# Kernel optimization log

Measured on AMD Instinct MI355X. Metric: run time of the kernel, lower is better.

## Reference

```python
import jax, jax.numpy as jnp
import numpy as np

H, HS, C = 16, 64, 1024  # num_heads, head_size, n_embd

def setup_inputs() -> dict:
    key = jax.random.key(0)
    ks = jax.random.split(key, 5)
    B, T = 2, 2048
    s = 1.0 / np.sqrt(C)
    return {
        "x": jax.random.normal(ks[0], (B, T, C), dtype=jnp.float32),
        "Wq": jax.random.normal(ks[1], (H, C, HS), dtype=jnp.float32) * s,
        "Wk": jax.random.normal(ks[2], (H, C, HS), dtype=jnp.float32) * s,
        "Wv": jax.random.normal(ks[3], (H, C, HS), dtype=jnp.float32) * s,
        "Wo": jax.random.normal(ks[4], (C, C), dtype=jnp.float32) * s,
    }

def reference(x, Wq, Wk, Wv, Wo):
    B, T, Cdim = x.shape
    scale = Cdim ** -0.5  # original scales by n_embd**-0.5, not head_size
    q = jnp.einsum('btc,hcd->bhtd', x, Wq)
    k = jnp.einsum('btc,hcd->bhtd', x, Wk)
    v = jnp.einsum('btc,hcd->bhtd', x, Wv)
    wei = jnp.einsum('bhtd,bhsd->bhts', q, k) * scale  # [B,H,T,T]
    causal = jnp.tril(jnp.ones((T, T), dtype=bool))
    wei = jnp.where(causal, wei, -jnp.inf)
    wei = jax.nn.softmax(wei, axis=-1)
    out = jnp.einsum('bhts,bhsd->bhtd', wei, v)  # [B,H,T,HS]
    out = out.transpose(0, 2, 1, 3).reshape(B, T, -1)  # concat heads -> [B,T,C]
    return out @ Wo.T
```

## Files before the change

kernel.cpp:

```cpp
#include <hip/hip_runtime.h>

typedef unsigned short ushort_t;
typedef __bf16 bf16x8 __attribute__((ext_vector_type(8)));
typedef float f32x4 __attribute__((ext_vector_type(4)));
typedef float f32x16 __attribute__((ext_vector_type(16)));
typedef unsigned short ushortx8 __attribute__((ext_vector_type(8)));
typedef unsigned int uintx4 __attribute__((ext_vector_type(4)));

#define NH 16
#define HS 64
#define CD 1024
#define NB 2
#define NT 2048
#define BT (NB * NT)
#define N3 (3 * CD)

#define L2E_DIV32 0.04508422002778011f

#define PART1_OFF 50331648
#define SLOT_BYTES 18432
#define R0_SLOTS 796


__device__ __forceinline__ ushort_t bf16_rne(float f) {
  union { float f; unsigned u; } v; v.f = f;
  unsigned u = v.u;
  unsigned r = (u + 0x7FFFu + ((u >> 16) & 1u)) >> 16;
  return (ushort_t)r;
}

__device__ __forceinline__ float bf2f(ushort_t u) {
  union { unsigned u; float f; } v; v.u = ((unsigned)u) << 16; return v.f;
}

__device__ __forceinline__ void gload_lds16(const ushort_t* g, ushort_t* l) {
  __builtin_amdgcn_global_load_lds(
      (const __attribute__((address_space(1))) unsigned int*)g,
      (__attribute__((address_space(3))) unsigned int*)l, 16, 0, 0);
}

__device__ __forceinline__ f32x4 mfma16(ushortx8 a, ushortx8 b, f32x4 c) {
  return __builtin_amdgcn_mfma_f32_16x16x32_bf16(
      __builtin_bit_cast(bf16x8, a), __builtin_bit_cast(bf16x8, b), c, 0, 0, 0);
}

__device__ __forceinline__ f32x16 mfma32(ushortx8 a, ushortx8 b, f32x16 c) {
  return __builtin_amdgcn_mfma_f32_32x32x16_bf16(
      __builtin_bit_cast(bf16x8, a), __builtin_bit_cast(bf16x8, b), c, 0, 0, 0);
}

__device__ __forceinline__ unsigned cvt_pk_bf16(float lo, float hi) {
  unsigned r;
  asm("v_cvt_pk_bf16_f32 %0, %1, %2" : "=v"(r) : "v"(lo), "v"(hi));
  return r;
}

__device__ __forceinline__ void plswap(unsigned &a, unsigned &b) {
  asm volatile("v_permlane32_swap_b32 %0, %1" : "+v"(a), "+v"(b));
}


__global__ __launch_bounds__(256)
void pack_cast(const float4* __restrict__ in, ushort_t* __restrict__ out, int n4) {
  const int i = blockIdx.x * 256 + threadIdx.x;
  if (i >= n4) return;
  const float4 v = in[i];
  ushort4 r;
  r.x = bf16_rne(v.x); r.y = bf16_rne(v.y);
  r.z = bf16_rne(v.z); r.w = bf16_rne(v.w);
  *(ushort4*)(out + (size_t)i * 4) = r;
}

__global__ __launch_bounds__(256)
void pack_wqkv(const float* __restrict__ Wq, const float* __restrict__ Wk,
               const float* __restrict__ Wv, ushort_t* __restrict__ out) {
  __shared__ ushort_t tile[64 * 66];
  const int sh = blockIdx.y;
  const int s = sh >> 4, h = sh & 15;
  const float* W = (s == 0) ? Wq : ((s == 1) ? Wk : Wv);
  const int c0 = blockIdx.x * 64;
  const int t = threadIdx.x;
#pragma unroll
  for (int j = 0; j < 16; ++j) {
    const int idx = t + j * 256;
    const int ci = idx >> 6, d = idx & 63;
    const float v = W[(size_t)(h * 1024 + c0 + ci) * 64 + d];
    tile[d * 66 + ci] = bf16_rne(v);
  }
  __syncthreads();
#pragma unroll
  for (int j = 0; j < 16; ++j) {
    const int idx = t + j * 256;
    const int d = idx >> 6, ci = idx & 63;
    out[(size_t)(s * 1024 + h * 64 + d) * 1024 + c0 + ci] = tile[d * 66 + ci];
  }
}


template <bool OUT_BF16>
__global__ __launch_bounds__(256)
void gemm_bt(const ushort_t* __restrict__ A, const ushort_t* __restrict__ Bt,
             void* __restrict__ Cv, int M, int N, int K, int qcols) {
  __shared__ __align__(16) ushort_t ldsA[2][128 * 32];
  __shared__ __align__(16) ushort_t ldsB[2][128 * 32];
  const int tid = threadIdx.x;
  const int lane = tid & 63;
  const int wave = tid >> 6;
  const int row0 = blockIdx.y * 128;
  const int col0 = blockIdx.x * 128;
  const int wm = wave >> 1, wn = wave & 1;
  const float sc = (col0 < qcols) ? L2E_DIV32 : 1.0f;

  f32x4 acc[4][4] = {};

  const int ce = (tid & 3) * 8;

  auto stage = [&](int buf, int kt) {
    const int kbase = kt * 32;
#pragma unroll
    for (int j = 0; j < 2; ++j) {
      const int r = j * 64 + (tid >> 2);
      gload_lds16(A + (size_t)(row0 + r) * K + kbase + ce,
                  &ldsA[buf][(j * 256 + wave * 64) * 8]);
      gload_lds16(Bt + (size_t)(col0 + r) * K + kbase + ce,
                  &ldsB[buf][(j * 256 + wave * 64) * 8]);
    }
  };

  const int arow_off = (wm * 64 + (lane & 15)) * 32 + (lane >> 4) * 8;
  const int brow_off = (wn * 64 + (lane & 15)) * 32 + (lane >> 4) * 8;

  auto compute = [&](int buf) {
    ushortx8 af[4], bfr[4];
#pragma unroll
    for (int m = 0; m < 4; ++m)
      af[m] = *(const ushortx8*)&ldsA[buf][arow_off + m * 512];
#pragma unroll
    for (int n = 0; n < 4; ++n)
      bfr[n] = *(const ushortx8*)&ldsB[buf][brow_off + n * 512];
#pragma unroll
    for (int m = 0; m < 4; ++m)
#pragma unroll
      for (int n = 0; n < 4; ++n)
        acc[m][n] = mfma16(af[m], bfr[n], acc[m][n]);
  };

  stage(0, 0);
  __syncthreads();
  const int nk = K >> 5;
  for (int kt = 0; kt < nk; ++kt) {
    const int cur = kt & 1;
    if (kt + 1 < nk) stage(cur ^ 1, kt + 1);
    compute(cur);
    __syncthreads();
  }

#pragma unroll
  for (int m = 0; m < 4; ++m) {
    const int rbase = row0 + wm * 64 + m * 16 + (lane >> 4) * 4;
#pragma unroll
    for (int n = 0; n < 4; ++n) {
      const int col = col0 + wn * 64 + n * 16 + (lane & 15);
#pragma unroll
      for (int i = 0; i < 4; ++i) {
        const size_t off = (size_t)(rbase + i) * N + col;
        if constexpr (OUT_BF16) ((ushort_t*)Cv)[off] = bf16_rne(acc[m][n][i] * sc);
        else                    ((float*)Cv)[off]    = acc[m][n][i] * sc;
      }
    }
  }
}


__global__ __launch_bounds__(256, 4)
void attn_fwd4(const ushort_t* __restrict__ QKV, ushort_t* __restrict__ O,
               char* __restrict__ wsb) {
  __shared__ __align__(16) ushort_t Klds[2][64 * 64];
  __shared__ __align__(16) ushort_t Vlds[2][64 * 64];

  const int tid = threadIdx.x;
  const int lane = tid & 63;
  const int w = tid >> 6;
  const int l31 = lane & 31;
  const int h = lane >> 5;

  const int x = blockIdx.x;
  const int bh = x & 31;
  const int c = x >> 5;
  int qb, j, k;
  if (c < 16)      { qb = 12 + (c >> 2); j = c & 3; k = 4; }
  else if (c < 28) { const int e = c - 16; const int q = e / 3; qb = 8 + q; j = e - q * 3; k = 3; }
  else if (c < 36) { const int e = c - 28; qb = 4 + (e >> 1); j = e & 1; k = 2; }
  else             { qb = c - 36; j = 0; k = 1; }
  const int nt = 2 * qb + 2;
  const int bsz = nt / k, rem = nt - bsz * k;
  const int t0 = j * bsz + (j < rem ? j : rem);
  const int t1 = t0 + bsz + (j < rem ? 1 : 0);
  const bool lastc = (t1 == nt);

  const int b = bh >> 4, head = bh & 15;
  const size_t base = (size_t)b * NT * N3;
  const int qw0 = qb * 128 + w * 32;
  const int qg = qw0 + l31;
  const int tmax = lastc ? (2 * qb + (w >> 1)) : (t1 - 1);

  ushortx8 qf[4];
  {
    const ushort_t* qp = QKV + base + (size_t)qg * N3 + head * 64 + h * 8;
#pragma unroll
    for (int kc = 0; kc < 4; ++kc) qf[kc] = *(const ushortx8*)(qp + kc * 16);
  }

  int koff[4];
#pragma unroll
  for (int kc = 0; kc < 4; ++kc)
    koff[kc] = l31 * 128 + (((2 * kc + h) ^ (l31 & 7)) * 16);

  const int vr = l31, vc = w * 2 + h;
  int voff[8];
#pragma unroll
  for (int e = 0; e < 8; ++e)
    voff[e] = (vc * 8 + e) * 128 + (((vr >> 2) ^ e) * 16) + 4 * (vr & 3);

  const int rowA = tid >> 3, ccA = tid & 7;
  const int rowB = 32 + rowA;
  const ushort_t* kg = QKV + base + 1024 + head * 64;
  const ushort_t* ksA = kg + (size_t)(t0 * 64 + rowA) * N3 + ((ccA ^ (rowA & 7)) * 8);
  const ushort_t* ksB = kg + (size_t)(t0 * 64 + rowB) * N3 + ((ccA ^ (rowB & 7)) * 8);
  const ushort_t* vs  = QKV + base + (size_t)(t0 * 64 + 2 * vr) * N3 + 2048 + head * 64 + vc * 8;
  const size_t tadv = (size_t)64 * N3;

  f32x16 oA = {}, oB = {};
  float m_r = -INFINITY, l_r = 0.f;

  ushortx8 vst0 = *(const ushortx8*)vs;
  ushortx8 vst1 = *(const ushortx8*)(vs + N3);
  gload_lds16(ksA, &Klds[0][(w * 64) * 8]);
  gload_lds16(ksB, &Klds[0][(256 + w * 64) * 8]);
#pragma unroll
  for (int e = 0; e < 8; ++e) {
    ushort2 val; val.x = vst0[e]; val.y = vst1[e];
    *(ushort2*)((char*)&Vlds[0][0] + voff[e]) = val;
  }
  asm volatile("s_waitcnt lgkmcnt(0)" ::: "memory");

  int curb = 0;
  for (int t = t0; t < t1; ++t) {
    const bool hasn = (t + 1 < t1);
    const int nxt = curb ^ 1;
    if (hasn) {
      ksA += tadv; ksB += tadv; vs += tadv;
      vst0 = *(const ushortx8*)vs;
      vst1 = *(const ushortx8*)(vs + N3);
      gload_lds16(ksA, &Klds[nxt][(w * 64) * 8]);
      gload_lds16(ksB, &Klds[nxt][(256 + w * 64) * 8]);
      asm volatile("s_waitcnt vmcnt(4)" ::: "memory");
    } else {
      asm volatile("s_waitcnt vmcnt(0)" ::: "memory");
    }
    __builtin_amdgcn_s_barrier();
    asm volatile("" ::: "memory");

    if (t <= tmax) {
      const bool diag = lastc && (t == tmax);
      const bool halfB = diag && ((w & 1) == 0);
      const char* kb = (const char*)&Klds[curb][0];
      const char* vb = (const char*)&Vlds[curb][0];

      f32x16 sA = {}, sB = {};
#pragma unroll
      for (int kc = 0; kc < 4; ++kc)
        sA = mfma32(*(const ushortx8*)(kb + koff[kc]), qf[kc], sA);
      if (!halfB) {
#pragma unroll
        for (int kc = 0; kc < 4; ++kc)
          sB = mfma32(*(const ushortx8*)(kb + 4096 + koff[kc]), qf[kc], sB);
      }

      if (diag) {
#pragma unroll
        for (int r = 0; r < 16; ++r) {
          const int krow = (r & 3) + 8 * (r >> 2) + 4 * h;
          if (halfB) { if (krow > l31) sA[r] = -INFINITY; }
          else       { if (krow > l31) sB[r] = -INFINITY; }
        }
      }

      float mm[16];
#pragma unroll
      for (int r = 0; r < 16; ++r) mm[r] = halfB ? sA[r] : fmaxf(sA[r], sB[r]);
#pragma unroll
      for (int st = 8; st >= 1; st >>= 1)
#pragma unroll
        for (int r = 0; r < st; ++r) mm[r] = fmaxf(mm[r], mm[r + st]);
      const float mx = fmaxf(mm[0], __shfl_xor(mm[0], 32, 64));

      if (__any(mx > m_r + 8.0f)) {
        const float mn = fmaxf(m_r, mx);
        const float al = exp2f(m_r - mn);
        m_r = mn; l_r *= al;
#pragma unroll
        for (int r = 0; r < 16; ++r) { oA[r] *= al; oB[r] *= al; }
      }

      unsigned u[16];
      float ps[8];
#pragma unroll
      for (int jj = 0; jj < 8; ++jj) {
        const float e0 = exp2f(sA[2 * jj] - m_r);
        const float e1 = exp2f(sA[2 * jj + 1] - m_r);
        u[jj] = cvt_pk_bf16(e0, e1);
        ps[jj] = e0 + e1;
      }
      if (!halfB) {
#pragma unroll
        for (int jj = 0; jj < 8; ++jj) {
          const float e0 = exp2f(sB[2 * jj] - m_r);
          const float e1 = exp2f(sB[2 * jj + 1] - m_r);
          u[8 + jj] = cvt_pk_bf16(e0, e1);
          ps[jj] += e0 + e1;
        }
      }
#pragma unroll
      for (int st = 4; st >= 1; st >>= 1)
#pragma unroll
        for (int r = 0; r < st; ++r) ps[r] += ps[r + st];
      l_r += ps[0] + __shfl_xor(ps[0], 32, 64);

      plswap(u[0], u[2]);   plswap(u[1], u[3]);
      plswap(u[4], u[6]);   plswap(u[5], u[7]);
      if (!halfB) {
        plswap(u[8], u[10]);  plswap(u[9], u[11]);
        plswap(u[12], u[14]); plswap(u[13], u[15]);
      }

#pragma unroll
      for (int kc = 0; kc < 4; ++kc) {
        if (kc < 2 || !halfB) {
          uintx4 pw;
          pw[0] = u[4 * kc + 0]; pw[1] = u[4 * kc + 1];
          pw[2] = u[4 * kc + 2]; pw[3] = u[4 * kc + 3];
          const ushortx8 pav = __builtin_bit_cast(ushortx8, pw);
          oA = mfma32(*(const ushortx8*)(vb + koff[kc]), pav, oA);
          oB = mfma32(*(const ushortx8*)(vb + 4096 + koff[kc]), pav, oB);
        }
      }
    }

    if (hasn) {
#pragma unroll
      for (int e = 0; e < 8; ++e) {
        ushort2 val; val.x = vst0[e]; val.y = vst1[e];
        *(ushort2*)((char*)&Vlds[nxt][0] + voff[e]) = val;
      }
    }
    asm volatile("s_waitcnt lgkmcnt(0)" ::: "memory");
    __builtin_amdgcn_s_barrier();
    asm volatile("" ::: "memory");
    curb ^= 1;
  }

  if (k == 1) {
    const float inv_l = 1.0f / l_r;
    ushort_t* op = O + ((size_t)(b * NT + qg)) * 1024 + head * 64;
#pragma unroll
    for (int db = 0; db < 2; ++db)
#pragma unroll
      for (int g = 0; g < 4; ++g) {
        ushort4 pk;
        pk.x = bf16_rne((db ? oB[4 * g + 0] : oA[4 * g + 0]) * inv_l);
        pk.y = bf16_rne((db ? oB[4 * g + 1] : oA[4 * g + 1]) * inv_l);
        pk.z = bf16_rne((db ? oB[4 * g + 2] : oA[4 * g + 2]) * inv_l);
        pk.w = bf16_rne((db ? oB[4 * g + 3] : oA[4 * g + 3]) * inv_l);
        *(ushort4*)(op + db * 32 + 8 * g + 4 * h) = pk;
      }
  } else {
    const int local = (qb < 8) ? ((qb - 4) * 2 + j)
                    : (qb < 12) ? (8 + (qb - 8) * 3 + j)
                    : (20 + (qb - 12) * 4 + j);
    const int s = bh * 36 + local;
    char* wb = (s < R0_SLOTS ? wsb + (size_t)s * SLOT_BYTES
                             : wsb + PART1_OFF + (size_t)(s - R0_SLOTS) * SLOT_BYTES)
               + w * 4608;
#pragma unroll
    for (int g = 0; g < 4; ++g) {
      ushortx8 pk;
#pragma unroll
      for (int e2 = 0; e2 < 8; ++e2)
        pk[e2] = bf16_rne(g < 2 ? oA[g * 8 + e2] : oB[(g - 2) * 8 + e2]);
      *(ushortx8*)(wb + lane * 64 + g * 16) = pk;
    }
    *(float*)(wb + 4096 + lane * 4) = m_r;
    *(float*)(wb + 4352 + lane * 4) = l_r;
  }
}

__global__ __launch_bounds__(256)
void attn_merge(const char* __restrict__ wsb, ushort_t* __restrict__ O) {
  const int x = blockIdx.x;
  const int bh = x & 31;
  const int qi = x >> 5;
  const int qb = 4 + qi;
  const int k  = qi < 4 ? 2 : (qi < 8 ? 3 : 4);
  const int lb = qi < 4 ? qi * 2 : (qi < 8 ? 8 + (qi - 4) * 3 : 20 + (qi - 8) * 4);
  const int tid = threadIdx.x;
  const int lane = tid & 63;
  const int w = tid >> 6;
  const int l31 = lane & 31;
  const int h = lane >> 5;

  const char* wbs[4];
  float mj[4], lj[4];
  float M = -INFINITY;
#pragma unroll
  for (int jj = 0; jj < 4; ++jj) {
    if (jj < k) {
      const int s = bh * 36 + lb + jj;
      const char* wb = (s < R0_SLOTS ? wsb + (size_t)s * SLOT_BYTES
                                     : wsb + PART1_OFF + (size_t)(s - R0_SLOTS) * SLOT_BYTES)
                       + w * 4608;
      wbs[jj] = wb;
      mj[jj] = *(const float*)(wb + 4096 + lane * 4);
      lj[jj] = *(const float*)(wb + 4352 + lane * 4);
      M = fmaxf(M, mj[jj]);
    }
  }
  float o[32];
#pragma unroll
  for (int r = 0; r < 32; ++r) o[r] = 0.f;
  float lacc = 0.f;
#pragma unroll
  for (int jj = 0; jj < 4; ++jj) {
    if (jj < k) {
      const float a = exp2f(mj[jj] - M);
      lacc += a * lj[jj];
#pragma unroll
      for (int g = 0; g < 4; ++g) {
        const ushortx8 v = *(const ushortx8*)(wbs[jj] + lane * 64 + g * 16);
#pragma unroll
        for (int e = 0; e < 8; ++e) o[g * 8 + e] += a * bf2f(v[e]);
      }
    }
  }
  const float inv_l = 1.0f / lacc;
  const int b = bh >> 4, head = bh & 15;
  const int qg = qb * 128 + w * 32 + l31;
  ushort_t* op = O + ((size_t)(b * NT + qg)) * 1024 + head * 64;
#pragma unroll
  for (int db = 0; db < 2; ++db)
#pragma unroll
    for (int g = 0; g < 4; ++g) {
      ushort4 pk;
      pk.x = bf16_rne(o[db * 16 + 4 * g + 0] * inv_l);
      pk.y = bf16_rne(o[db * 16 + 4 * g + 1] * inv_l);
      pk.z = bf16_rne(o[db * 16 + 4 * g + 2] * inv_l);
      pk.w = bf16_rne(o[db * 16 + 4 * g + 3] * inv_l);
      *(ushort4*)(op + db * 32 + 8 * g + 4 * h) = pk;
    }
}


extern "C" void kernel_launch(void* const* d_in, const int* in_sizes, int n_in,
                              void* d_out, int out_size, void* d_ws, size_t ws_size,
                              hipStream_t stream) {
  (void)in_sizes; (void)n_in; (void)out_size; (void)ws_size;
  const float* x  = (const float*)d_in[0];
  const float* Wq = (const float*)d_in[1];
  const float* Wk = (const float*)d_in[2];
  const float* Wv = (const float*)d_in[3];
  const float* Wo = (const float*)d_in[4];

  char* ws = (char*)d_ws;
  ushort_t* Xbf    = (ushort_t*)(ws);
  ushort_t* Wqkv_t = (ushort_t*)(ws + 8388608);
  ushort_t* Wo_bf  = (ushort_t*)(ws + 14680064);
  ushort_t* QKV    = (ushort_t*)(ws + 16777216);
  ushort_t* Obf    = (ushort_t*)(ws + 41943040);

  pack_cast<<<4096, 256, 0, stream>>>((const float4*)x, Xbf, 1048576);
  pack_cast<<<1024, 256, 0, stream>>>((const float4*)Wo, Wo_bf, 262144);
  pack_wqkv<<<dim3(16, 48), 256, 0, stream>>>(Wq, Wk, Wv, Wqkv_t);

  gemm_bt<true><<<dim3(24, 32), 256, 0, stream>>>(Xbf, Wqkv_t, QKV, BT, N3, CD, 1024);
  attn_fwd4<<<1280, 256, 0, stream>>>(QKV, Obf, ws);
  attn_merge<<<384, 256, 0, stream>>>(ws, Obf);
  gemm_bt<false><<<dim3(8, 32), 256, 0, stream>>>(Obf, Wo_bf, d_out, BT, CD, CD, 0);
}
```

Baseline: 147.7 us.

## Write V transposed from QKV GEMM epilogue and stream it into LDS asynchronously

The QKV projection epilogue now writes V in a per-head transposed layout [B*C, T] and keeps Q/K in a narrower 2048-wide buffer. The attention kernel then loads V tiles with direct global-to-LDS loads, the same way it loads K, instead of register loads followed by scattered LDS writes and an extra lgkmcnt wait. This removes per-iteration V shuffle work and register pressure, so launch bounds are raised to 5 blocks per CU. The cost is strided 8-byte stores in the GEMM epilogue for the V columns, and the workspace must now fit the Vt region without overlapping the partial-result slots.

```diff
diff --git a/kernel.cpp b/kernel.cpp
--- a/kernel.cpp
+++ b/kernel.cpp
@@ -17,8 +17,10 @@
 
 #define L2E_DIV32 0.04508422002778011f
 
+#define QKV_LD 2048
 #define PART1_OFF 50331648
 #define SLOT_BYTES 18432
+#define WAVE_BYTES 4608
 #define R0_SLOTS 796
 
 
@@ -97,10 +99,11 @@
 }
 
 
-template <bool OUT_BF16>
+template <int MODE>
 __global__ __launch_bounds__(256)
 void gemm_bt(const ushort_t* __restrict__ A, const ushort_t* __restrict__ Bt,
-             void* __restrict__ Cv, int M, int N, int K, int qcols) {
+             void* __restrict__ Cv, ushort_t* __restrict__ Vt,
+             int M, int N, int K) {
   __shared__ __align__(16) ushort_t ldsA[2][128 * 32];
   __shared__ __align__(16) ushort_t ldsB[2][128 * 32];
   const int tid = threadIdx.x;
@@ -109,7 +112,6 @@
   const int row0 = blockIdx.y * 128;
   const int col0 = blockIdx.x * 128;
   const int wm = wave >> 1, wn = wave & 1;
-  const float sc = (col0 < qcols) ? L2E_DIV32 : 1.0f;
 
   f32x4 acc[4][4] = {};
 
@@ -161,20 +163,37 @@
 #pragma unroll
     for (int n = 0; n < 4; ++n) {
       const int col = col0 + wn * 64 + n * 16 + (lane & 15);
-#pragma unroll
-      for (int i = 0; i < 4; ++i) {
-        const size_t off = (size_t)(rbase + i) * N + col;
-        if constexpr (OUT_BF16) ((ushort_t*)Cv)[off] = bf16_rne(acc[m][n][i] * sc);
-        else                    ((float*)Cv)[off]    = acc[m][n][i] * sc;
-      }
-    }
-  }
-}
-
-
-__global__ __launch_bounds__(256, 4)
-void attn_fwd4(const ushort_t* __restrict__ QKV, ushort_t* __restrict__ O,
-               char* __restrict__ wsb) {
+      if constexpr (MODE == 0) {
+#pragma unroll
+        for (int i = 0; i < 4; ++i)
+          ((float*)Cv)[(size_t)(rbase + i) * N + col] = acc[m][n][i];
+      } else {
+        if (col < 2048) {
+          const float sc = (col < 1024) ? L2E_DIV32 : 1.0f;
+#pragma unroll
+          for (int i = 0; i < 4; ++i)
+            ((ushort_t*)Cv)[(size_t)(rbase + i) * QKV_LD + col] =
+                bf16_rne(acc[m][n][i] * sc);
+        } else {
+          const int dcol = col - 2048;
+          const int bI = rbase >> 11;
+          const int t0i = rbase & 2047;
+          ushort4 pk;
+          pk.x = bf16_rne(acc[m][n][0]);
+          pk.y = bf16_rne(acc[m][n][1]);
+          pk.z = bf16_rne(acc[m][n][2]);
+          pk.w = bf16_rne(acc[m][n][3]);
+          *(ushort4*)(Vt + (size_t)(bI * 1024 + dcol) * NT + t0i) = pk;
+        }
+      }
+    }
+  }
+}
+
+
+__global__ __launch_bounds__(256, 5)
+void attn_fwd6(const ushort_t* __restrict__ QKV, const ushort_t* __restrict__ Vt,
+               ushort_t* __restrict__ O, char* __restrict__ wsb) {
   __shared__ __align__(16) ushort_t Klds[2][64 * 64];
   __shared__ __align__(16) ushort_t Vlds[2][64 * 64];
 
@@ -199,61 +218,51 @@
   const bool lastc = (t1 == nt);
 
   const int b = bh >> 4, head = bh & 15;
-  const size_t base = (size_t)b * NT * N3;
-  const int qw0 = qb * 128 + w * 32;
-  const int qg = qw0 + l31;
+  const size_t base = (size_t)b * NT * QKV_LD;
+  const int qg = qb * 128 + w * 32 + l31;
   const int tmax = lastc ? (2 * qb + (w >> 1)) : (t1 - 1);
 
   ushortx8 qf[4];
   {
-    const ushort_t* qp = QKV + base + (size_t)qg * N3 + head * 64 + h * 8;
+    const ushort_t* qp = QKV + base + (size_t)qg * QKV_LD + head * 64 + h * 8;
 #pragma unroll
     for (int kc = 0; kc < 4; ++kc) qf[kc] = *(const ushortx8*)(qp + kc * 16);
   }
+  asm volatile("s_waitcnt vmcnt(0)" ::: "memory");
 
   int koff[4];
 #pragma unroll
   for (int kc = 0; kc < 4; ++kc)
     koff[kc] = l31 * 128 + (((2 * kc + h) ^ (l31 & 7)) * 16);
-
-  const int vr = l31, vc = w * 2 + h;
-  int voff[8];
-#pragma unroll
-  for (int e = 0; e < 8; ++e)
-    voff[e] = (vc * 8 + e) * 128 + (((vr >> 2) ^ e) * 16) + 4 * (vr & 3);
 
   const int rowA = tid >> 3, ccA = tid & 7;
   const int rowB = 32 + rowA;
   const ushort_t* kg = QKV + base + 1024 + head * 64;
-  const ushort_t* ksA = kg + (size_t)(t0 * 64 + rowA) * N3 + ((ccA ^ (rowA & 7)) * 8);
-  const ushort_t* ksB = kg + (size_t)(t0 * 64 + rowB) * N3 + ((ccA ^ (rowB & 7)) * 8);
-  const ushort_t* vs  = QKV + base + (size_t)(t0 * 64 + 2 * vr) * N3 + 2048 + head * 64 + vc * 8;
-  const size_t tadv = (size_t)64 * N3;
+  const ushort_t* vg = Vt + (size_t)(bh * 64) * NT;
+  const ushort_t* ksA = kg + (size_t)(t0 * 64 + rowA) * QKV_LD + ((ccA ^ (rowA & 7)) * 8);
+  const ushort_t* ksB = kg + (size_t)(t0 * 64 + rowB) * QKV_LD + ((ccA ^ (rowB & 7)) * 8);
+  const ushort_t* vsA = vg + (size_t)rowA * NT + t0 * 64 + ((ccA ^ (rowA & 7)) * 8);
+  const ushort_t* vsB = vg + (size_t)rowB * NT + t0 * 64 + ((ccA ^ (rowB & 7)) * 8);
+  const size_t kadv = (size_t)64 * QKV_LD;
 
   f32x16 oA = {}, oB = {};
   float m_r = -INFINITY, l_r = 0.f;
 
-  ushortx8 vst0 = *(const ushortx8*)vs;
-  ushortx8 vst1 = *(const ushortx8*)(vs + N3);
   gload_lds16(ksA, &Klds[0][(w * 64) * 8]);
   gload_lds16(ksB, &Klds[0][(256 + w * 64) * 8]);
-#pragma unroll
-  for (int e = 0; e < 8; ++e) {
-    ushort2 val; val.x = vst0[e]; val.y = vst1[e];
-    *(ushort2*)((char*)&Vlds[0][0] + voff[e]) = val;
-  }
-  asm volatile("s_waitcnt lgkmcnt(0)" ::: "memory");
+  gload_lds16(vsA, &Vlds[0][(w * 64) * 8]);
+  gload_lds16(vsB, &Vlds[0][(256 + w * 64) * 8]);
 
   int curb = 0;
   for (int t = t0; t < t1; ++t) {
     const bool hasn = (t + 1 < t1);
     const int nxt = curb ^ 1;
     if (hasn) {
-      ksA += tadv; ksB += tadv; vs += tadv;
-      vst0 = *(const ushortx8*)vs;
-      vst1 = *(const ushortx8*)(vs + N3);
+      ksA += kadv; ksB += kadv; vsA += 64; vsB += 64;
       gload_lds16(ksA, &Klds[nxt][(w * 64) * 8]);
       gload_lds16(ksB, &Klds[nxt][(256 + w * 64) * 8]);
+      gload_lds16(vsA, &Vlds[nxt][(w * 64) * 8]);
+      gload_lds16(vsB, &Vlds[nxt][(256 + w * 64) * 8]);
       asm volatile("s_waitcnt vmcnt(4)" ::: "memory");
     } else {
       asm volatile("s_waitcnt vmcnt(0)" ::: "memory");
@@ -347,14 +356,6 @@
       }
     }
 
-    if (hasn) {
-#pragma unroll
-      for (int e = 0; e < 8; ++e) {
-        ushort2 val; val.x = vst0[e]; val.y = vst1[e];
-        *(ushort2*)((char*)&Vlds[nxt][0] + voff[e]) = val;
-      }
-    }
-    asm volatile("s_waitcnt lgkmcnt(0)" ::: "memory");
     __builtin_amdgcn_s_barrier();
     asm volatile("" ::: "memory");
     curb ^= 1;
@@ -381,7 +382,7 @@
     const int s = bh * 36 + local;
     char* wb = (s < R0_SLOTS ? wsb + (size_t)s * SLOT_BYTES
                              : wsb + PART1_OFF + (size_t)(s - R0_SLOTS) * SLOT_BYTES)
-               + w * 4608;
+               + w * WAVE_BYTES;
 #pragma unroll
     for (int g = 0; g < 4; ++g) {
       ushortx8 pk;
@@ -418,7 +419,7 @@
       const int s = bh * 36 + lb + jj;
       const char* wb = (s < R0_SLOTS ? wsb + (size_t)s * SLOT_BYTES
                                      : wsb + PART1_OFF + (size_t)(s - R0_SLOTS) * SLOT_BYTES)
-                       + w * 4608;
+                       + w * WAVE_BYTES;
       wbs[jj] = wb;
       mj[jj] = *(const float*)(wb + 4096 + lane * 4);
       lj[jj] = *(const float*)(wb + 4352 + lane * 4);
@@ -475,14 +476,15 @@
   ushort_t* Wqkv_t = (ushort_t*)(ws + 8388608);
   ushort_t* Wo_bf  = (ushort_t*)(ws + 14680064);
   ushort_t* QKV    = (ushort_t*)(ws + 16777216);
+  ushort_t* Vt     = (ushort_t*)(ws + 33554432);
   ushort_t* Obf    = (ushort_t*)(ws + 41943040);
 
   pack_cast<<<4096, 256, 0, stream>>>((const float4*)x, Xbf, 1048576);
   pack_cast<<<1024, 256, 0, stream>>>((const float4*)Wo, Wo_bf, 262144);
   pack_wqkv<<<dim3(16, 48), 256, 0, stream>>>(Wq, Wk, Wv, Wqkv_t);
 
-  gemm_bt<true><<<dim3(24, 32), 256, 0, stream>>>(Xbf, Wqkv_t, QKV, BT, N3, CD, 1024);
-  attn_fwd4<<<1280, 256, 0, stream>>>(QKV, Obf, ws);
+  gemm_bt<1><<<dim3(24, 32), 256, 0, stream>>>(Xbf, Wqkv_t, QKV, Vt, BT, N3, CD);
+  attn_fwd6<<<1280, 256, 0, stream>>>(QKV, Vt, Obf, ws);
   attn_merge<<<384, 256, 0, stream>>>(ws, Obf);
-  gemm_bt<false><<<dim3(8, 32), 256, 0, stream>>>(Obf, Wo_bf, d_out, BT, CD, CD, 0);
-}
+  gemm_bt<0><<<dim3(8, 32), 256, 0, stream>>>(Obf, Wo_bf, d_out, nullptr, BT, CD, CD);
+}
```

After: 225.7 us. 1.53x slower.
